# Kernel tuning notes

Measured on AMD Instinct MI355X. Metric: run time of the kernel, lower is better.

The kernel has to match this reference:

```python
import jax, jax.numpy as jnp
import numpy as np

OVERFLOW_MARGIN = 1e-08

N, D, OUT = 8192, 128, 128


def setup_inputs() -> dict:
    key = jax.random.key(0)
    k1, k2, k3 = jax.random.split(key, 3)
    values = jax.random.normal(k1, (N, D), dtype=jnp.float32)
    adjacency = jax.random.uniform(k2, (N, N), dtype=jnp.float32)
    W = jax.random.normal(k3, (D, OUT), dtype=jnp.float32) * 0.05
    b = jnp.zeros((OUT,), dtype=jnp.float32)
    return {"values": values, "adjacency": adjacency, "W": W, "b": b}


def reference(values, adjacency, W, b):
    # Dense projection: fc_sc = values @ W + b  -> [N, OUT]
    fc_sc = values @ W + b
    # degree d = A @ ones -> row sums, [N]
    d = jnp.sum(adjacency, axis=1)
    d_inv_sqrt = 1.0 / (jnp.sqrt(d) + OVERFLOW_MARGIN)  # [N]
    # laplacian = diag(d_inv_sqrt) @ A @ diag(d_inv_sqrt)
    # expressed as row/col broadcast scaling (same math, no NxN diag matmuls)
    laplacian = adjacency * d_inv_sqrt[:, None] * d_inv_sqrt[None, :]
    # graph conv: [N,N] @ [N,OUT]
    return laplacian @ fc_sc
```

## Files before the change

### kernel.cpp

```cpp
#include <hip/hip_runtime.h>

#define NROWS 8192
#define DIM   128
#define RS    132
#define PSTR  520

typedef __attribute__((ext_vector_type(8))) short  short8;
typedef __attribute__((ext_vector_type(4))) float  floatx4;

__device__ __forceinline__ unsigned pk_bf16(float a, float b) {
  unsigned ua = __float_as_uint(a);
  ua += 0x7fffu + ((ua >> 16) & 1u);
  unsigned ub = __float_as_uint(b);
  ub += 0x7fffu + ((ub >> 16) & 1u);
  return (ua >> 16) | (ub & 0xffff0000u);
}

__global__ __launch_bounds__(256) void k_prep(const float* __restrict__ A,
                                              float* __restrict__ d,
                                              unsigned short* __restrict__ Abf) {
  __shared__ unsigned short B[16 * PSTR];
  __shared__ float rsum[16 * 17];
  int iblk = blockIdx.x;
  int wb   = blockIdx.y;
  int i0   = iblk * 16;
  int jwin = wb * 512;
  int t = threadIdx.x;
  int r = t >> 4, l16 = t & 15;

  const float* ap = A + (size_t)(i0 + r) * NROWS + jwin + l16 * 8;
  float sum = 0.f;
#pragma unroll
  for (int it = 0; it < 4; ++it) {
    float4 lo = *(const float4*)(ap + it * 128);
    float4 hi = *(const float4*)(ap + it * 128 + 4);
    sum += (lo.x + lo.y) + (lo.z + lo.w) + (hi.x + hi.y) + (hi.z + hi.w);
    uint4 p = make_uint4(pk_bf16(lo.x, lo.y), pk_bf16(lo.z, lo.w),
                         pk_bf16(hi.x, hi.y), pk_bf16(hi.z, hi.w));
    *(uint4*)&B[r * PSTR + l16 * 8 + it * 128] = p;
  }
  rsum[r * 17 + l16] = sum;
  __syncthreads();
  if (t < 16) {
    float s2 = 0.f;
#pragma unroll
    for (int c = 0; c < 16; ++c) s2 += rsum[t * 17 + c];
    atomicAdd(&d[i0 + t], s2);
  }
  int jb = t >> 4, p = t & 15;
  unsigned short* tbase = Abf + ((size_t)iblk * 256 + wb * 16 + jb) * 512;
#pragma unroll
  for (int q = 0; q < 4; ++q) {
    uint4 v = *(const uint4*)&B[p * PSTR + jb * 32 + q * 8];
    *(uint4*)(tbase + (size_t)(q * 16 + p) * 8) = v;
  }
}

__global__ __launch_bounds__(256) void k_sconv(const float* __restrict__ d,
                                               float* __restrict__ s) {
  int i = blockIdx.x * 256 + threadIdx.x;
  s[i] = 1.0f / (sqrtf(d[i]) + 1e-8f);
}

__global__ __launch_bounds__(256) void k_fc(const float* __restrict__ V,
                                            const float* __restrict__ W,
                                            const float* __restrict__ b,
                                            const float* __restrict__ s,
                                            unsigned short* __restrict__ gTt) {
  __shared__ float Wl[DIM * DIM];
  __shared__ float Vl[32 * DIM];
  __shared__ unsigned short Fl[32 * DIM];
  int r0 = blockIdx.x * 32;
  {
    const float4* Wg = (const float4*)W;
    float4* Wd = (float4*)Wl;
#pragma unroll
    for (int i = 0; i < DIM * DIM / 4 / 256; ++i)
      Wd[threadIdx.x + i * 256] = Wg[threadIdx.x + i * 256];
    const float4* Vg = (const float4*)(V + (size_t)r0 * DIM);
    float4* Vd = (float4*)Vl;
#pragma unroll
    for (int i = 0; i < 32 * DIM / 4 / 256; ++i)
      Vd[threadIdx.x + i * 256] = Vg[threadIdx.x + i * 256];
  }
  __syncthreads();

  int cg = threadIdx.x & 31;
  int rg = threadIdx.x >> 5;
  float acc[4][4] = {};
  for (int dd = 0; dd < DIM; ++dd) {
    float4 w = *(const float4*)&Wl[dd * DIM + cg * 4];
#pragma unroll
    for (int rr = 0; rr < 4; ++rr) {
      float v = Vl[(rg * 4 + rr) * DIM + dd];
      acc[rr][0] += v * w.x; acc[rr][1] += v * w.y;
      acc[rr][2] += v * w.z; acc[rr][3] += v * w.w;
    }
  }
  float bb[4], sv[4];
#pragma unroll
  for (int cc = 0; cc < 4; ++cc) bb[cc] = b[cg * 4 + cc];
#pragma unroll
  for (int rr = 0; rr < 4; ++rr) sv[rr] = s[r0 + rg * 4 + rr];
#pragma unroll
  for (int rr = 0; rr < 4; ++rr)
#pragma unroll
    for (int cc = 0; cc < 4; cc += 2) {
      unsigned p = pk_bf16((acc[rr][cc]     + bb[cc])     * sv[rr],
                           (acc[rr][cc + 1] + bb[cc + 1]) * sv[rr]);
      *(unsigned*)&Fl[(rg * 4 + rr) * DIM + cg * 4 + cc] = p;
    }
  __syncthreads();

  int kblk = threadIdx.x >> 5, s5 = threadIdx.x & 31;
  int jblk = r0 >> 5;
#pragma unroll
  for (int h = 0; h < 2; ++h) {
    int L = s5 + h * 32;
    int l15 = L & 15, quad = L >> 4;
    int k = kblk * 16 + l15;
    unsigned w0 = (unsigned)Fl[(quad * 8 + 0) * DIM + k] | ((unsigned)Fl[(quad * 8 + 1) * DIM + k] << 16);
    unsigned w1 = (unsigned)Fl[(quad * 8 + 2) * DIM + k] | ((unsigned)Fl[(quad * 8 + 3) * DIM + k] << 16);
    unsigned w2 = (unsigned)Fl[(quad * 8 + 4) * DIM + k] | ((unsigned)Fl[(quad * 8 + 5) * DIM + k] << 16);
    unsigned w3 = (unsigned)Fl[(quad * 8 + 6) * DIM + k] | ((unsigned)Fl[(quad * 8 + 7) * DIM + k] << 16);
    *(uint4*)(gTt + ((size_t)(kblk * 256 + jblk) * 64 + L) * 8) = make_uint4(w0, w1, w2, w3);
  }
}

__global__ __launch_bounds__(256, 4) void k_spmm(const unsigned short* __restrict__ Abf,
                                                 const unsigned short* __restrict__ gTt,
                                                 float* __restrict__ partial) {
  __shared__ float red[4 * 32 * RS];
  int t = threadIdx.x, w = t >> 6, lane = t & 63;
  int bi = blockIdx.x >> 2, ks = blockIdx.x & 3;
  int jblk0 = ks * 64 + w * 16;

  const unsigned short* ab = Abf + ((size_t)bi * 2 * 256 + jblk0) * 512 + lane * 8;
  const unsigned short* gb = gTt + (size_t)jblk0 * 512 + lane * 8;

  floatx4 acc[8][2];
#pragma unroll
  for (int kb = 0; kb < 8; ++kb)
#pragma unroll
    for (int ib = 0; ib < 2; ++ib)
      acc[kb][ib] = (floatx4){0.f, 0.f, 0.f, 0.f};

#pragma unroll 2
  for (int it = 0; it < 16; ++it) {
    short8 af0 = *(const short8*)(ab);
    short8 af1 = *(const short8*)(ab + (size_t)256 * 512);
    short8 gf[8];
#pragma unroll
    for (int kb = 0; kb < 8; ++kb)
      gf[kb] = *(const short8*)(gb + (size_t)kb * 256 * 512);
#pragma unroll
    for (int kb = 0; kb < 8; ++kb) {
      acc[kb][0] = __builtin_amdgcn_mfma_f32_16x16x32_bf16(gf[kb], af0, acc[kb][0], 0, 0, 0);
      acc[kb][1] = __builtin_amdgcn_mfma_f32_16x16x32_bf16(gf[kb], af1, acc[kb][1], 0, 0, 0);
    }
    ab += 512; gb += 512;
  }

  int l15 = lane & 15, quad = lane >> 4;
  float* myred = red + w * 32 * RS;
#pragma unroll
  for (int ib = 0; ib < 2; ++ib)
#pragma unroll
    for (int kb = 0; kb < 8; ++kb) {
      float4 v = make_float4(acc[kb][ib][0], acc[kb][ib][1], acc[kb][ib][2], acc[kb][ib][3]);
      *(float4*)(myred + (ib * 16 + l15) * RS + kb * 16 + quad * 4) = v;
    }
  __syncthreads();

  int ii = t >> 3, kg = (t & 7) * 16;
  float4 sum[4];
#pragma unroll
  for (int c = 0; c < 4; ++c) sum[c] = make_float4(0.f, 0.f, 0.f, 0.f);
#pragma unroll
  for (int ww = 0; ww < 4; ++ww)
#pragma unroll
    for (int c = 0; c < 4; ++c) {
      float4 v = *(const float4*)(red + ww * 32 * RS + ii * RS + kg + c * 4);
      sum[c].x += v.x; sum[c].y += v.y; sum[c].z += v.z; sum[c].w += v.w;
    }
  float* pout = partial + ((size_t)(ks * 256 + bi) * 32 + ii) * 128 + kg;
#pragma unroll
  for (int c = 0; c < 4; ++c) *(float4*)(pout + c * 4) = sum[c];
}

__global__ __launch_bounds__(256) void k_reduce(const float* __restrict__ partial,
                                                const float* __restrict__ s,
                                                float* __restrict__ out) {
  int g = blockIdx.x * 256 + threadIdx.x;
  int i = g >> 5, c4 = (g & 31) * 4;
  size_t base = (size_t)i * 128 + c4;
  const size_t kstr = (size_t)256 * 32 * 128;
  float4 a = *(const float4*)(partial + base);
  float4 bq = *(const float4*)(partial + base + kstr);
  float4 c = *(const float4*)(partial + base + 2 * kstr);
  float4 dq = *(const float4*)(partial + base + 3 * kstr);
  float si = s[i];
  float4 r;
  r.x = si * (a.x + bq.x + c.x + dq.x);
  r.y = si * (a.y + bq.y + c.y + dq.y);
  r.z = si * (a.z + bq.z + c.z + dq.z);
  r.w = si * (a.w + bq.w + c.w + dq.w);
  *(float4*)(out + base) = r;
}

extern "C" void kernel_launch(void* const* d_in, const int* in_sizes, int n_in,
                              void* d_out, int out_size, void* d_ws, size_t ws_size,
                              hipStream_t stream) {
  const float* values    = (const float*)d_in[0];
  const float* adjacency = (const float*)d_in[1];
  const float* W         = (const float*)d_in[2];
  const float* b         = (const float*)d_in[3];
  float* out = (float*)d_out;

  char* ws = (char*)d_ws;
  float* d            = (float*)ws;
  float* s            = (float*)(ws + 32768);
  unsigned short* gTt = (unsigned short*)(ws + 65536);
  float* partial      = (float*)(ws + 65536 + 2097152);
  unsigned short* Abf = (unsigned short*)(ws + 33554432);

  hipMemsetAsync(d, 0, NROWS * sizeof(float), stream);
  k_prep<<<dim3(512, 16), 256, 0, stream>>>(adjacency, d, Abf);
  k_sconv<<<NROWS / 256, 256, 0, stream>>>(d, s);
  k_fc<<<NROWS / 32, 256, 0, stream>>>(values, W, b, s, gTt);
  k_spmm<<<1024, 256, 0, stream>>>(Abf, gTt, partial);
  k_reduce<<<NROWS * 32 / 256, 256, 0, stream>>>(partial, s, out);
}
```

Baseline: 449.7 us.

## Split spmm waves over output columns and fold inverse-sqrt into consumers

```diff
diff --git a/kernel.cpp b/kernel.cpp
--- a/kernel.cpp
+++ b/kernel.cpp
@@ -2,7 +2,6 @@
 
 #define NROWS 8192
 #define DIM   128
-#define RS    132
 #define PSTR  520
 
 typedef __attribute__((ext_vector_type(8))) short  short8;
@@ -14,6 +13,10 @@
   unsigned ub = __float_as_uint(b);
   ub += 0x7fffu + ((ub >> 16) & 1u);
   return (ua >> 16) | (ub & 0xffff0000u);
+}
+
+__device__ __forceinline__ float inv_sqrt_d(float dv) {
+  return 1.0f / (sqrtf(dv) + 1e-8f);
 }
 
 __global__ __launch_bounds__(256) void k_prep(const float* __restrict__ A,
@@ -56,16 +59,10 @@
   }
 }
 
-__global__ __launch_bounds__(256) void k_sconv(const float* __restrict__ d,
-                                               float* __restrict__ s) {
-  int i = blockIdx.x * 256 + threadIdx.x;
-  s[i] = 1.0f / (sqrtf(d[i]) + 1e-8f);
-}
-
 __global__ __launch_bounds__(256) void k_fc(const float* __restrict__ V,
                                             const float* __restrict__ W,
                                             const float* __restrict__ b,
-                                            const float* __restrict__ s,
+                                            const float* __restrict__ d,
                                             unsigned short* __restrict__ gTt) {
   __shared__ float Wl[DIM * DIM];
   __shared__ float Vl[32 * DIM];
@@ -101,7 +98,7 @@
 #pragma unroll
   for (int cc = 0; cc < 4; ++cc) bb[cc] = b[cg * 4 + cc];
 #pragma unroll
-  for (int rr = 0; rr < 4; ++rr) sv[rr] = s[r0 + rg * 4 + rr];
+  for (int rr = 0; rr < 4; ++rr) sv[rr] = inv_sqrt_d(d[r0 + rg * 4 + rr]);
 #pragma unroll
   for (int rr = 0; rr < 4; ++rr)
 #pragma unroll
@@ -127,79 +124,61 @@
   }
 }
 
-__global__ __launch_bounds__(256, 4) void k_spmm(const unsigned short* __restrict__ Abf,
+__global__ __launch_bounds__(256, 8) void k_spmm(const unsigned short* __restrict__ Abf,
                                                  const unsigned short* __restrict__ gTt,
                                                  float* __restrict__ partial) {
-  __shared__ float red[4 * 32 * RS];
   int t = threadIdx.x, w = t >> 6, lane = t & 63;
   int bi = blockIdx.x >> 2, ks = blockIdx.x & 3;
-  int jblk0 = ks * 64 + w * 16;
-
-  const unsigned short* ab = Abf + ((size_t)bi * 2 * 256 + jblk0) * 512 + lane * 8;
-  const unsigned short* gb = gTt + (size_t)jblk0 * 512 + lane * 8;
-
-  floatx4 acc[8][2];
-#pragma unroll
-  for (int kb = 0; kb < 8; ++kb)
-#pragma unroll
-    for (int ib = 0; ib < 2; ++ib)
-      acc[kb][ib] = (floatx4){0.f, 0.f, 0.f, 0.f};
-
-#pragma unroll 2
-  for (int it = 0; it < 16; ++it) {
-    short8 af0 = *(const short8*)(ab);
-    short8 af1 = *(const short8*)(ab + (size_t)256 * 512);
-    short8 gf[8];
-#pragma unroll
-    for (int kb = 0; kb < 8; ++kb)
-      gf[kb] = *(const short8*)(gb + (size_t)kb * 256 * 512);
-#pragma unroll
-    for (int kb = 0; kb < 8; ++kb) {
-      acc[kb][0] = __builtin_amdgcn_mfma_f32_16x16x32_bf16(gf[kb], af0, acc[kb][0], 0, 0, 0);
-      acc[kb][1] = __builtin_amdgcn_mfma_f32_16x16x32_bf16(gf[kb], af1, acc[kb][1], 0, 0, 0);
+  int kb0 = w * 2;
+
+  const unsigned short* ab = Abf + (((size_t)(2 * bi) * 256 + ks * 64) * 64 + lane) * 8;
+  const unsigned short* gb = gTt + (((size_t)kb0 * 256 + ks * 64) * 64 + lane) * 8;
+  const size_t TSTR = 256 * 512;
+
+  floatx4 acc[2][2];
+#pragma unroll
+  for (int ib = 0; ib < 2; ++ib)
+#pragma unroll
+    for (int kb = 0; kb < 2; ++kb)
+      acc[ib][kb] = (floatx4){0.f, 0.f, 0.f, 0.f};
+
+#pragma unroll 4
+  for (int jb = 0; jb < 64; ++jb) {
+    short8 a0 = *(const short8*)(ab);
+    short8 a1 = *(const short8*)(ab + TSTR);
+    short8 g0 = *(const short8*)(gb);
+    short8 g1 = *(const short8*)(gb + TSTR);
+    acc[0][0] = __builtin_amdgcn_mfma_f32_16x16x32_bf16(g0, a0, acc[0][0], 0, 0, 0);
+    acc[0][1] = __builtin_amdgcn_mfma_f32_16x16x32_bf16(g1, a0, acc[0][1], 0, 0, 0);
+    acc[1][0] = __builtin_amdgcn_mfma_f32_16x16x32_bf16(g0, a1, acc[1][0], 0, 0, 0);
+    acc[1][1] = __builtin_amdgcn_mfma_f32_16x16x32_bf16(g1, a1, acc[1][1], 0, 0, 0);
+    ab += 512; gb += 512;
+  }
+
+  int l15 = lane & 15, quad = lane >> 4;
+#pragma unroll
+  for (int ib = 0; ib < 2; ++ib)
+#pragma unroll
+    for (int kb = 0; kb < 2; ++kb) {
+      float* p = partial + ((size_t)(ks * 256 + bi) * 32 + ib * 16 + l15) * 128
+                         + (kb0 + kb) * 16 + quad * 4;
+      *(float4*)p = make_float4(acc[ib][kb][0], acc[ib][kb][1],
+                                acc[ib][kb][2], acc[ib][kb][3]);
     }
-    ab += 512; gb += 512;
-  }
-
-  int l15 = lane & 15, quad = lane >> 4;
-  float* myred = red + w * 32 * RS;
-#pragma unroll
-  for (int ib = 0; ib < 2; ++ib)
-#pragma unroll
-    for (int kb = 0; kb < 8; ++kb) {
-      float4 v = make_float4(acc[kb][ib][0], acc[kb][ib][1], acc[kb][ib][2], acc[kb][ib][3]);
-      *(float4*)(myred + (ib * 16 + l15) * RS + kb * 16 + quad * 4) = v;
-    }
-  __syncthreads();
-
-  int ii = t >> 3, kg = (t & 7) * 16;
-  float4 sum[4];
-#pragma unroll
-  for (int c = 0; c < 4; ++c) sum[c] = make_float4(0.f, 0.f, 0.f, 0.f);
-#pragma unroll
-  for (int ww = 0; ww < 4; ++ww)
-#pragma unroll
-    for (int c = 0; c < 4; ++c) {
-      float4 v = *(const float4*)(red + ww * 32 * RS + ii * RS + kg + c * 4);
-      sum[c].x += v.x; sum[c].y += v.y; sum[c].z += v.z; sum[c].w += v.w;
-    }
-  float* pout = partial + ((size_t)(ks * 256 + bi) * 32 + ii) * 128 + kg;
-#pragma unroll
-  for (int c = 0; c < 4; ++c) *(float4*)(pout + c * 4) = sum[c];
 }
 
 __global__ __launch_bounds__(256) void k_reduce(const float* __restrict__ partial,
-                                                const float* __restrict__ s,
+                                                const float* __restrict__ d,
                                                 float* __restrict__ out) {
   int g = blockIdx.x * 256 + threadIdx.x;
   int i = g >> 5, c4 = (g & 31) * 4;
   size_t base = (size_t)i * 128 + c4;
   const size_t kstr = (size_t)256 * 32 * 128;
-  float4 a = *(const float4*)(partial + base);
+  float4 a  = *(const float4*)(partial + base);
   float4 bq = *(const float4*)(partial + base + kstr);
-  float4 c = *(const float4*)(partial + base + 2 * kstr);
+  float4 c  = *(const float4*)(partial + base + 2 * kstr);
   float4 dq = *(const float4*)(partial + base + 3 * kstr);
-  float si = s[i];
+  float si = inv_sqrt_d(d[i]);
   float4 r;
   r.x = si * (a.x + bq.x + c.x + dq.x);
   r.y = si * (a.y + bq.y + c.y + dq.y);
@@ -219,15 +198,13 @@
 
   char* ws = (char*)d_ws;
   float* d            = (float*)ws;
-  float* s            = (float*)(ws + 32768);
   unsigned short* gTt = (unsigned short*)(ws + 65536);
   float* partial      = (float*)(ws + 65536 + 2097152);
   unsigned short* Abf = (unsigned short*)(ws + 33554432);
 
   hipMemsetAsync(d, 0, NROWS * sizeof(float), stream);
   k_prep<<<dim3(512, 16), 256, 0, stream>>>(adjacency, d, Abf);
-  k_sconv<<<NROWS / 256, 256, 0, stream>>>(d, s);
-  k_fc<<<NROWS / 32, 256, 0, stream>>>(values, W, b, s, gTt);
+  k_fc<<<NROWS / 32, 256, 0, stream>>>(values, W, b, d, gTt);
   k_spmm<<<1024, 256, 0, stream>>>(Abf, gTt, partial);
-  k_reduce<<<NROWS * 32 / 256, 256, 0, stream>>>(partial, s, out);
-}
+  k_reduce<<<NROWS * 32 / 256, 256, 0, stream>>>(partial, d, out);
+}
```

Result: no change. 456.0 us (+1.4%).
